# Kernel tuning notes

Hardware: AMD Instinct MI355X
Metric: run time of the kernel (lower is better)

Reference implementation:

```python
import jax, jax.numpy as jnp
import numpy as np

B, S, D, H = 64, 512, 512, 1024


def setup_inputs() -> dict:
    key = jax.random.key(0)
    ks = jax.random.split(key, 11)
    s = lambda fan_in: 1.0 / np.sqrt(fan_in)
    return {
        "x": jax.random.normal(ks[0], (B, S, D), dtype=jnp.float32),
        # gate: Linear(D+H -> H), stored as (in, out)
        "Wg": jax.random.uniform(ks[1], (D + H, H), jnp.float32, -s(D + H), s(D + H)),
        "bg": jax.random.uniform(ks[2], (H,), jnp.float32, -s(D + H), s(D + H)),
        # GRUCell: input->hidden (D, 3H), hidden->hidden (H, 3H), chunks [r|z|n]
        "W_ih": jax.random.uniform(ks[3], (D, 3 * H), jnp.float32, -s(H), s(H)),
        "b_ih": jax.random.uniform(ks[4], (3 * H,), jnp.float32, -s(H), s(H)),
        "W_hh": jax.random.uniform(ks[5], (H, 3 * H), jnp.float32, -s(H), s(H)),
        "b_hh": jax.random.uniform(ks[6], (3 * H,), jnp.float32, -s(H), s(H)),
        # attention_layer: Linear(2H -> H)
        "Wa": jax.random.uniform(ks[7], (2 * H, H), jnp.float32, -s(2 * H), s(2 * H)),
        "ba": jax.random.uniform(ks[8], (H,), jnp.float32, -s(2 * H), s(2 * H)),
        # attention_score: Linear(H -> 1)
        "Ws": jax.random.uniform(ks[9], (H, 1), jnp.float32, -s(H), s(H)),
        "bs": jax.random.uniform(ks[10], (1,), jnp.float32, -s(H), s(H)),
    }


def reference(x, Wg, bg, W_ih, b_ih, W_hh, b_hh, Wa, ba, Ws, bs):
    h0 = jnp.zeros((x.shape[0], W_hh.shape[0]), dtype=x.dtype)  # [B, H]
    xs = jnp.swapaxes(x, 0, 1)  # [S, B, D] for scan over time

    def step(h, xt):
        # selective gate on [x_t, h_{t-1}]
        g = jax.nn.sigmoid(jnp.concatenate([xt, h], axis=-1) @ Wg + bg)
        # GRUCell (PyTorch semantics)
        gi = xt @ W_ih + b_ih          # [B, 3H]
        gh = h @ W_hh + b_hh           # [B, 3H]
        ir, iz, inn = jnp.split(gi, 3, axis=-1)
        hr, hz, hn = jnp.split(gh, 3, axis=-1)
        r = jax.nn.sigmoid(ir + hr)
        z = jax.nn.sigmoid(iz + hz)
        n = jnp.tanh(inn + r * hn)
        h_new = (1.0 - z) * n + z * h
        h_new = g * h_new
        # per-step attention gating (softmax over a size-1 axis, as in source)
        att_h = jnp.tanh(jnp.concatenate([h_new, h_new], axis=-1) @ Wa + ba)
        score = att_h @ Ws + bs        # [B, 1]
        att_w = jax.nn.softmax(score, axis=1)
        h_new = h_new * att_w
        return h_new, None

    h_last, _ = jax.lax.scan(step, h0, xs)
    return h_last  # outputs[:, -1, :]
```

## Files before the change

### kernel.cpp

```cpp
#include <hip/hip_runtime.h>

typedef _Float16 half8 __attribute__((ext_vector_type(8)));
typedef float f32x4 __attribute__((ext_vector_type(4)));
typedef unsigned uint4v __attribute__((ext_vector_type(4)));

#define BB 64
#define SS 512
#define DD 512
#define HH 1024
#define KK 1536
#define GG 4
#define RR 16
#define PKST 48

#define MFMA(a, b, c) __builtin_amdgcn_mfma_f32_16x16x32_f16(a, b, c, 0, 0, 0)

__device__ __host__ __forceinline__ int kperm(int k) {
  int blk = k >> 5, r = k & 31;
  return (blk << 5) | (((r >> 2) & 3) << 3) | ((r >> 4) << 2) | (r & 3);
}

__global__ void prep_w(const float* __restrict__ Wg, const float* __restrict__ Wih,
                       const float* __restrict__ Whh, _Float16* __restrict__ Wp) {
  int p = blockIdx.x;
  int b = p / 80, rem = p % 80, t = rem >> 4, c = rem & 15;
  int j = b * 16 + c;
  for (int pass = 0; pass < 6; ++pass) {
    int k = pass * 256 + threadIdx.x;
    float v;
    if (t == 0)      v = Wg[k * HH + j];
    else if (t == 1) v = (k < DD) ? Wih[k * 3 * HH + j]          : Whh[(k - DD) * 3 * HH + j];
    else if (t == 2) v = (k < DD) ? Wih[k * 3 * HH + HH + j]     : Whh[(k - DD) * 3 * HH + HH + j];
    else if (t == 3) v = (k < DD) ? Wih[k * 3 * HH + 2 * HH + j] : 0.f;
    else             v = (k < DD) ? 0.f : Whh[(k - DD) * 3 * HH + 2 * HH + j];
    int pos = (k < DD) ? kperm(k) : k;
    Wp[(size_t)p * KK + pos] = (_Float16)v;
  }
}

__global__ void prep_xh(const float* __restrict__ x, _Float16* __restrict__ Xh) {
  int t = blockIdx.x, sg = blockIdx.y;
  int row = threadIdx.x >> 2, lkg = threadIdx.x & 3;
  const float* xp = x + ((size_t)row * SS + t) * DD + sg * 32 + lkg * 4;
  half8 hv;
#pragma unroll
  for (int j = 0; j < 4; ++j) { hv[j] = (_Float16)xp[j]; hv[4 + j] = (_Float16)xp[16 + j]; }
  *(half8*)(Xh + ((((size_t)t * 16 + sg) * 64 + row) * 4 + lkg) * 8) = hv;
}

#define WAITV(lit) do { asm volatile("s_waitcnt vmcnt(" lit ")" ::: "memory"); \
                        __builtin_amdgcn_sched_barrier(0); } while (0)


__device__ __forceinline__ void issue_pk2(const uint4v* ap, uint4v& P0, uint4v& P1) {
  asm volatile("global_load_dwordx4 %0, %2, off sc0 sc1\n\t"
               "global_load_dwordx4 %1, %2, off offset:16 sc0 sc1"
               : "=&v"(P0), "=&v"(P1) : "v"(ap) : "memory");
}

__device__ __forceinline__ int tags_ok2(const uint4v& P0, const uint4v& P1, unsigned want) {
  return __all((int)(((P0[3] ^ want) | (P1[3] ^ want)) == 0));
}

#define RETRY2(P0a, P1a, ap_) do { \
    if (!tags_ok2(P0a, P1a, want)) { \
      do { issue_pk2(ap_, P0a, P1a); WAITV("0"); } \
      while (!tags_ok2(P0a, P1a, want)); } } while (0)

__global__ __launch_bounds__(512, 2) void rnn_seq(
    const _Float16* __restrict__ Xh, const _Float16* __restrict__ Wp,
    const float* __restrict__ bg, const float* __restrict__ bih,
    const float* __restrict__ bhh, float* __restrict__ out,
    uint4v* __restrict__ Pk) {
  const int blk = blockIdx.x;
  const int g = blk >> 6;
  const int cb = blk & 63;
  const int tid = threadIdx.x;
  const int w = tid >> 6;
  const int lane = tid & 63;
  const int lrow = lane & 15;
  const int lkg = lane >> 4;
  const int phalf = lkg >> 1;
  const int odd = lkg & 1;
  const int wk = (w + cb) & 7;
  const int pk_off = 3 * lrow + odd;

  __shared__ float Red[8][80][18];
  __shared__ alignas(16) _Float16 Xstage[16 * 512];

  const int ej = tid & 15;
  const int rr = (tid >> 4) & 15;
  const int ghcol = cb * 16 + ej;
  const float bg_b  = bg[ghcol];
  const float br_b  = bih[ghcol] + bhh[ghcol];
  const float bz_b  = bih[HH + ghcol] + bhh[HH + ghcol];
  const float bin_b = bih[2 * HH + ghcol];
  const float bhn_b = bhh[2 * HH + ghcol];
  float hreg = 0.f;

  const int pbase = wk * 8 + phalf;

  half8 bx[3][2], b3[2], bh[3][4], b4[4];
#pragma unroll
  for (int tt = 0; tt < 3; ++tt)
#pragma unroll
    for (int kk = 0; kk < 2; ++kk)
      bx[tt][kk] = *(const half8*)(Wp + (size_t)(cb * 80 + tt * 16 + lrow) * KK + (w * 2 + kk) * 32 + lkg * 8);
#pragma unroll
  for (int kk = 0; kk < 2; ++kk)
    b3[kk] = *(const half8*)(Wp + (size_t)(cb * 80 + 48 + lrow) * KK + (w * 2 + kk) * 32 + lkg * 8);
#pragma unroll
  for (int tt = 0; tt < 3; ++tt)
#pragma unroll
    for (int kk = 0; kk < 4; ++kk)
      bh[tt][kk] = *(const half8*)(Wp + (size_t)(cb * 80 + tt * 16 + lrow) * KK + (16 + wk * 4 + kk) * 32 + lkg * 8);
#pragma unroll
  for (int kk = 0; kk < 4; ++kk)
    b4[kk] = *(const half8*)(Wp + (size_t)(cb * 80 + 64 + lrow) * KK + (16 + wk * 4 + kk) * 32 + lkg * 8);

#pragma unroll
  for (int kk = 0; kk < 2; ++kk) {
    const _Float16* gsrc = Xh + ((((size_t)0 * 16 + (w * 2 + kk)) * 64 + (g * RR + lrow)) * 4 + lkg) * 8;
    __builtin_amdgcn_global_load_lds(
        (const __attribute__((address_space(1))) void*)gsrc,
        (__attribute__((address_space(3))) void*)(Xstage + (w * 2 + kk) * 512), 16, 0, 0);
  }
  WAITV("0");

  for (int t = 0; t < SS; ++t) {
    const uint4v* Rg = Pk + (size_t)((g * 2 + (t & 1)) * 64) * PKST;
    uint4v* Rn = Pk + (size_t)((g * 2 + ((t + 1) & 1)) * 64) * PKST;
    const unsigned want = (unsigned)t;
    const uint4v* apA = Rg + (size_t)(pbase + 0) * PKST + pk_off;
    const uint4v* apB = Rg + (size_t)(pbase + 2) * PKST + pk_off;
    const uint4v* apC = Rg + (size_t)(pbase + 4) * PKST + pk_off;
    const uint4v* apD = Rg + (size_t)(pbase + 6) * PKST + pk_off;

    f32x4 zz = {0.f, 0.f, 0.f, 0.f};
    f32x4 acc[5];
#pragma unroll
    for (int tt = 0; tt < 5; ++tt) acc[tt] = zz;

    half8 xfr[2];
#pragma unroll
    for (int kk = 0; kk < 2; ++kk)
      xfr[kk] = *(const half8*)(Xstage + (w * 2 + kk) * 512 + lane * 8);
    asm volatile("s_waitcnt lgkmcnt(0)" ::: "memory");
    __builtin_amdgcn_sched_barrier(0);

    {
      const int tn = (t + 1 < SS) ? t + 1 : t;
#pragma unroll
      for (int kk = 0; kk < 2; ++kk) {
        const _Float16* gsrc = Xh + ((((size_t)tn * 16 + (w * 2 + kk)) * 64 + (g * RR + lrow)) * 4 + lkg) * 8;
        __builtin_amdgcn_global_load_lds(
            (const __attribute__((address_space(1))) void*)gsrc,
            (__attribute__((address_space(3))) void*)(Xstage + (w * 2 + kk) * 512), 16, 0, 0);
      }
    }

    uint4v A0, A1, B0, B1, C0, C1, D0, D1;
    issue_pk2(apA, A0, A1);
    issue_pk2(apB, B0, B1);
    issue_pk2(apC, C0, C1);
    issue_pk2(apD, D0, D1);

#pragma unroll
    for (int kk = 0; kk < 2; ++kk) {
      acc[0] = MFMA(xfr[kk], bx[0][kk], acc[0]);
      acc[1] = MFMA(xfr[kk], bx[1][kk], acc[1]);
      acc[2] = MFMA(xfr[kk], bx[2][kk], acc[2]);
      acc[3] = MFMA(xfr[kk], b3[kk], acc[3]);
    }

    WAITV("6"); RETRY2(A0, A1, apA);
    {
      uint4v fv; fv[0] = odd ? A0[1] : A0[0]; fv[1] = odd ? A0[2] : A0[1];
      fv[2] = odd ? A1[0] : A0[2];     fv[3] = odd ? A1[1] : A1[0];
      half8 af = __builtin_bit_cast(half8, fv);
      acc[0] = MFMA(af, bh[0][0], acc[0]); acc[1] = MFMA(af, bh[1][0], acc[1]);
      acc[2] = MFMA(af, bh[2][0], acc[2]); acc[4] = MFMA(af, b4[0], acc[4]);
    }
    WAITV("4"); RETRY2(B0, B1, apB);
    {
      uint4v fv; fv[0] = odd ? B0[1] : B0[0]; fv[1] = odd ? B0[2] : B0[1];
      fv[2] = odd ? B1[0] : B0[2];     fv[3] = odd ? B1[1] : B1[0];
      half8 af = __builtin_bit_cast(half8, fv);
      acc[0] = MFMA(af, bh[0][1], acc[0]); acc[1] = MFMA(af, bh[1][1], acc[1]);
      acc[2] = MFMA(af, bh[2][1], acc[2]); acc[4] = MFMA(af, b4[1], acc[4]);
    }
    WAITV("2"); RETRY2(C0, C1, apC);
    {
      uint4v fv; fv[0] = odd ? C0[1] : C0[0]; fv[1] = odd ? C0[2] : C0[1];
      fv[2] = odd ? C1[0] : C0[2];     fv[3] = odd ? C1[1] : C1[0];
      half8 af = __builtin_bit_cast(half8, fv);
      acc[0] = MFMA(af, bh[0][2], acc[0]); acc[1] = MFMA(af, bh[1][2], acc[1]);
      acc[2] = MFMA(af, bh[2][2], acc[2]); acc[4] = MFMA(af, b4[2], acc[4]);
    }
    WAITV("0"); RETRY2(D0, D1, apD);
    {
      uint4v fv; fv[0] = odd ? D0[1] : D0[0]; fv[1] = odd ? D0[2] : D0[1];
      fv[2] = odd ? D1[0] : D0[2];     fv[3] = odd ? D1[1] : D1[0];
      half8 af = __builtin_bit_cast(half8, fv);
      acc[0] = MFMA(af, bh[0][3], acc[0]); acc[1] = MFMA(af, bh[1][3], acc[1]);
      acc[2] = MFMA(af, bh[2][3], acc[2]); acc[4] = MFMA(af, b4[3], acc[4]);
    }

#pragma unroll
    for (int tt = 0; tt < 5; ++tt)
      *(f32x4*)&Red[w][tt * 16 + lrow][lkg * 4] = acc[tt];
    __syncthreads();

    if (tid < 256) {
      float s5[5];
#pragma unroll
      for (int g5 = 0; g5 < 5; ++g5) {
        float a = 0.f;
#pragma unroll
        for (int sl = 0; sl < 8; ++sl) a += Red[sl][g5 * 16 + ej][rr];
        s5[g5] = a;
      }
      float g_ = 1.f / (1.f + __expf(-(s5[0] + bg_b)));
      float r_ = 1.f / (1.f + __expf(-(s5[1] + br_b)));
      float z_ = 1.f / (1.f + __expf(-(s5[2] + bz_b)));
      float n_ = tanhf(s5[3] + bin_b + r_ * (s5[4] + bhn_b));
      float h = g_ * ((1.f - z_) * n_ + z_ * hreg);
      hreg = h;
      if (t == SS - 1) {
        out[(size_t)(g * RR + rr) * HH + ghcol] = h;
      } else {
        unsigned hbits = (unsigned)__builtin_bit_cast(unsigned short, (_Float16)h);
        unsigned nb = (unsigned)__shfl_down((int)hbits, 1);
        int d = (int)(hbits | (nb << 16));
        int qp = lane / 3, sseg = lane - qp * 3;
        int srcbase = (qp << 4) + sseg * 6;
        int d0 = __builtin_amdgcn_ds_bpermute((srcbase + 0) << 2, d);
        int d1 = __builtin_amdgcn_ds_bpermute((srcbase + 2) << 2, d);
        int d2 = __builtin_amdgcn_ds_bpermute((srcbase + 4) << 2, d);
        if (lane < 12) {
          uint4v pk;
          pk[0] = (unsigned)d0;
          pk[1] = (unsigned)d1;
          pk[2] = (sseg == 2) ? 0u : (unsigned)d2;
          pk[3] = (unsigned)(t + 1);
          uint4v* dst = Rn + (size_t)cb * PKST + (w * 12 + lane);
          asm volatile("global_store_dwordx4 %0, %1, off sc0 sc1" :: "v"(dst), "v"(pk) : "memory");
        }
      }
    }
    __syncthreads();
  }
}

extern "C" void kernel_launch(void* const* d_in, const int* in_sizes, int n_in,
                              void* d_out, int out_size, void* d_ws, size_t ws_size,
                              hipStream_t stream) {
  const float* x   = (const float*)d_in[0];
  const float* Wg  = (const float*)d_in[1];
  const float* bg  = (const float*)d_in[2];
  const float* Wih = (const float*)d_in[3];
  const float* bih = (const float*)d_in[4];
  const float* Whh = (const float*)d_in[5];
  const float* bhh = (const float*)d_in[6];
  float* out = (float*)d_out;

  char* ws = (char*)d_ws;
  _Float16* Wp = (_Float16*)ws;
  _Float16* Xh = (_Float16*)(ws + 15728640);
  uint4v*   Pk = (uint4v*)(ws + 15728640 + 33554432);

  hipMemsetAsync((void*)Pk, 0, 393216, stream);
  prep_w<<<5120, 256, 0, stream>>>(Wg, Wih, Whh, Wp);
  prep_xh<<<dim3(512, 16), 256, 0, stream>>>(x, Xh);
  rnn_seq<<<256, 512, 0, stream>>>(Xh, Wp, bg, bih, bhh, out, Pk);
}
```

Before: 1.358 ms.

## Double-buffer reduction scratch to drop trailing barrier; split packet loads

The LDS reduction buffer gets a parity dimension, so step t+1 can write its partial sums while step t is still being reduced. That removes the second __syncthreads per timestep from the serial recurrence. The packet fetch now uses two independent aligned 16-byte loads and a reworked lane shuffle, replacing the former offset:16 pair. This doubles the reduction buffer's LDS footprint and relies on the single remaining barrier being enough to prevent races across the parity buffers.

```diff
diff --git a/kernel.cpp b/kernel.cpp
--- a/kernel.cpp
+++ b/kernel.cpp
@@ -52,19 +52,20 @@
                         __builtin_amdgcn_sched_barrier(0); } while (0)
 
 
-__device__ __forceinline__ void issue_pk2(const uint4v* ap, uint4v& P0, uint4v& P1) {
+__device__ __forceinline__ void issue_pk2(const uint4v* ap0, const uint4v* ap1,
+                                          uint4v& P0, uint4v& P1) {
   asm volatile("global_load_dwordx4 %0, %2, off sc0 sc1\n\t"
-               "global_load_dwordx4 %1, %2, off offset:16 sc0 sc1"
-               : "=&v"(P0), "=&v"(P1) : "v"(ap) : "memory");
+               "global_load_dwordx4 %1, %3, off sc0 sc1"
+               : "=&v"(P0), "=&v"(P1) : "v"(ap0), "v"(ap1) : "memory");
 }
 
 __device__ __forceinline__ int tags_ok2(const uint4v& P0, const uint4v& P1, unsigned want) {
   return __all((int)(((P0[3] ^ want) | (P1[3] ^ want)) == 0));
 }
 
-#define RETRY2(P0a, P1a, ap_) do { \
+#define RETRY2(P0a, P1a, ap0_, ap1_) do { \
     if (!tags_ok2(P0a, P1a, want)) { \
-      do { issue_pk2(ap_, P0a, P1a); WAITV("0"); } \
+      do { issue_pk2(ap0_, ap1_, P0a, P1a); WAITV("0"); } \
       while (!tags_ok2(P0a, P1a, want)); } } while (0)
 
 __global__ __launch_bounds__(512, 2) void rnn_seq(
@@ -83,9 +84,10 @@
   const int phalf = lkg >> 1;
   const int odd = lkg & 1;
   const int wk = (w + cb) & 7;
-  const int pk_off = 3 * lrow + odd;
-
-  __shared__ float Red[8][80][18];
+  const int pk0 = 3 * lrow + (odd ? 2 : 0);
+  const int pk1 = 3 * lrow + 1;
+
+  __shared__ float Red[2][8][80][18];
   __shared__ alignas(16) _Float16 Xstage[16 * 512];
 
   const int ej = tid & 15;
@@ -131,10 +133,15 @@
     const uint4v* Rg = Pk + (size_t)((g * 2 + (t & 1)) * 64) * PKST;
     uint4v* Rn = Pk + (size_t)((g * 2 + ((t + 1) & 1)) * 64) * PKST;
     const unsigned want = (unsigned)t;
-    const uint4v* apA = Rg + (size_t)(pbase + 0) * PKST + pk_off;
-    const uint4v* apB = Rg + (size_t)(pbase + 2) * PKST + pk_off;
-    const uint4v* apC = Rg + (size_t)(pbase + 4) * PKST + pk_off;
-    const uint4v* apD = Rg + (size_t)(pbase + 6) * PKST + pk_off;
+    const int par = t & 1;
+    const uint4v* apA0 = Rg + (size_t)(pbase + 0) * PKST + pk0;
+    const uint4v* apA1 = Rg + (size_t)(pbase + 0) * PKST + pk1;
+    const uint4v* apB0 = Rg + (size_t)(pbase + 2) * PKST + pk0;
+    const uint4v* apB1 = Rg + (size_t)(pbase + 2) * PKST + pk1;
+    const uint4v* apC0 = Rg + (size_t)(pbase + 4) * PKST + pk0;
+    const uint4v* apC1 = Rg + (size_t)(pbase + 4) * PKST + pk1;
+    const uint4v* apD0 = Rg + (size_t)(pbase + 6) * PKST + pk0;
+    const uint4v* apD1 = Rg + (size_t)(pbase + 6) * PKST + pk1;
 
     f32x4 zz = {0.f, 0.f, 0.f, 0.f};
     f32x4 acc[5];
@@ -160,10 +167,10 @@
     }
 
     uint4v A0, A1, B0, B1, C0, C1, D0, D1;
-    issue_pk2(apA, A0, A1);
-    issue_pk2(apB, B0, B1);
-    issue_pk2(apC, C0, C1);
-    issue_pk2(apD, D0, D1);
+    issue_pk2(apA0, apA1, A0, A1);
+    issue_pk2(apB0, apB1, B0, B1);
+    issue_pk2(apC0, apC1, C0, C1);
+    issue_pk2(apD0, apD1, D0, D1);
 
 #pragma unroll
     for (int kk = 0; kk < 2; ++kk) {
@@ -173,34 +180,34 @@
       acc[3] = MFMA(xfr[kk], b3[kk], acc[3]);
     }
 
-    WAITV("6"); RETRY2(A0, A1, apA);
-    {
-      uint4v fv; fv[0] = odd ? A0[1] : A0[0]; fv[1] = odd ? A0[2] : A0[1];
-      fv[2] = odd ? A1[0] : A0[2];     fv[3] = odd ? A1[1] : A1[0];
+    WAITV("6"); RETRY2(A0, A1, apA0, apA1);
+    {
+      uint4v fv; fv[0] = odd ? A1[1] : A0[0]; fv[1] = odd ? A1[2] : A0[1];
+      fv[2] = odd ? A0[0] : A0[2];     fv[3] = odd ? A0[1] : A1[0];
       half8 af = __builtin_bit_cast(half8, fv);
       acc[0] = MFMA(af, bh[0][0], acc[0]); acc[1] = MFMA(af, bh[1][0], acc[1]);
       acc[2] = MFMA(af, bh[2][0], acc[2]); acc[4] = MFMA(af, b4[0], acc[4]);
     }
-    WAITV("4"); RETRY2(B0, B1, apB);
-    {
-      uint4v fv; fv[0] = odd ? B0[1] : B0[0]; fv[1] = odd ? B0[2] : B0[1];
-      fv[2] = odd ? B1[0] : B0[2];     fv[3] = odd ? B1[1] : B1[0];
+    WAITV("4"); RETRY2(B0, B1, apB0, apB1);
+    {
+      uint4v fv; fv[0] = odd ? B1[1] : B0[0]; fv[1] = odd ? B1[2] : B0[1];
+      fv[2] = odd ? B0[0] : B0[2];     fv[3] = odd ? B0[1] : B1[0];
       half8 af = __builtin_bit_cast(half8, fv);
       acc[0] = MFMA(af, bh[0][1], acc[0]); acc[1] = MFMA(af, bh[1][1], acc[1]);
       acc[2] = MFMA(af, bh[2][1], acc[2]); acc[4] = MFMA(af, b4[1], acc[4]);
     }
-    WAITV("2"); RETRY2(C0, C1, apC);
-    {
-      uint4v fv; fv[0] = odd ? C0[1] : C0[0]; fv[1] = odd ? C0[2] : C0[1];
-      fv[2] = odd ? C1[0] : C0[2];     fv[3] = odd ? C1[1] : C1[0];
+    WAITV("2"); RETRY2(C0, C1, apC0, apC1);
+    {
+      uint4v fv; fv[0] = odd ? C1[1] : C0[0]; fv[1] = odd ? C1[2] : C0[1];
+      fv[2] = odd ? C0[0] : C0[2];     fv[3] = odd ? C0[1] : C1[0];
       half8 af = __builtin_bit_cast(half8, fv);
       acc[0] = MFMA(af, bh[0][2], acc[0]); acc[1] = MFMA(af, bh[1][2], acc[1]);
       acc[2] = MFMA(af, bh[2][2], acc[2]); acc[4] = MFMA(af, b4[2], acc[4]);
     }
-    WAITV("0"); RETRY2(D0, D1, apD);
-    {
-      uint4v fv; fv[0] = odd ? D0[1] : D0[0]; fv[1] = odd ? D0[2] : D0[1];
-      fv[2] = odd ? D1[0] : D0[2];     fv[3] = odd ? D1[1] : D1[0];
+    WAITV("0"); RETRY2(D0, D1, apD0, apD1);
+    {
+      uint4v fv; fv[0] = odd ? D1[1] : D0[0]; fv[1] = odd ? D1[2] : D0[1];
+      fv[2] = odd ? D0[0] : D0[2];     fv[3] = odd ? D0[1] : D1[0];
       half8 af = __builtin_bit_cast(half8, fv);
       acc[0] = MFMA(af, bh[0][3], acc[0]); acc[1] = MFMA(af, bh[1][3], acc[1]);
       acc[2] = MFMA(af, bh[2][3], acc[2]); acc[4] = MFMA(af, b4[3], acc[4]);
@@ -208,7 +215,7 @@
 
 #pragma unroll
     for (int tt = 0; tt < 5; ++tt)
-      *(f32x4*)&Red[w][tt * 16 + lrow][lkg * 4] = acc[tt];
+      *(f32x4*)&Red[par][w][tt * 16 + lrow][lkg * 4] = acc[tt];
     __syncthreads();
 
     if (tid < 256) {
@@ -217,7 +224,7 @@
       for (int g5 = 0; g5 < 5; ++g5) {
         float a = 0.f;
 #pragma unroll
-        for (int sl = 0; sl < 8; ++sl) a += Red[sl][g5 * 16 + ej][rr];
+        for (int sl = 0; sl < 8; ++sl) a += Red[par][sl][g5 * 16 + ej][rr];
         s5[g5] = a;
       }
       float g_ = 1.f / (1.f + __expf(-(s5[0] + bg_b)));
@@ -248,7 +255,6 @@
         }
       }
     }
-    __syncthreads();
   }
 }
 
```

Result: slower. 2.322 ms (+70.9%).
